# Kernel optimization log

Measured on AMD Instinct MI355X. Metric: run time of the kernel, lower is better.

The kernel has to match this reference:

```python
import jax, jax.numpy as jnp
import numpy as np

D = 1024           # d_model
E = 8              # n_experts
H = 2752           # hidden = round_up64(round(1024 * 8/3))
N = 8192
ALPHA = 0.05       # load_balance_alpha
TEMP = 1.0         # router temperature


def setup_inputs() -> dict:
    key = jax.random.key(0)
    k0, k1, k2, k3, k4 = jax.random.split(key, 5)
    s_in = 1.0 / np.sqrt(D)   # kaiming-uniform-ish bound for Linear(in=D)
    s_h = 1.0 / np.sqrt(H)    # bound for down proj Linear(in=H)
    x = jax.random.normal(k0, (N, D), jnp.float32)
    Wg = jax.random.uniform(k1, (E, D), jnp.float32, -s_in, s_in)   # router weight [E, D]
    bg = jnp.zeros((E,), jnp.float32)                               # router bias
    Wu = jax.random.uniform(k2, (E, H, D), jnp.float32, -s_in, s_in)  # up_u weights (torch [out,in])
    Wv = jax.random.uniform(k3, (E, H, D), jnp.float32, -s_in, s_in)  # up_v weights
    Wd = jax.random.uniform(k4, (E, D, H), jnp.float32, -s_h, s_h)    # down weights
    return {"x": x, "Wg": Wg, "bg": bg, "Wu": Wu, "Wv": Wv, "Wd": Wd}


def reference(x, Wg, bg, Wu, Wv, Wd):
    # ---- Top-1 router (eval mode: no noise, temperature=1) ----
    logits = x @ Wg.T + bg                 # [N, E]
    logits_base = logits / TEMP
    probs = jax.nn.softmax(logits_base, axis=-1)
    top1_idx = jnp.argmax(logits_base, axis=-1)                          # [N]
    top1_p = jnp.take_along_axis(probs, top1_idx[:, None], axis=-1)[:, 0]  # [N]

    # Load-balance aux loss (both factors are no-grad in the torch code)
    me = jax.lax.stop_gradient(jnp.mean(jax.nn.one_hot(top1_idx, E, dtype=probs.dtype), axis=0))
    ce = jax.lax.stop_gradient(jnp.mean(probs, axis=0))
    aux = ALPHA * E * jnp.sum(me * ce)

    # ---- Dropless dispatch + per-expert SwiGLU + weighted combine ----
    # Loop over the small, fixed expert set; each token contributes only via
    # its selected expert (gate is zero elsewhere), matching masked dispatch.
    y = jnp.zeros_like(x)
    for e in range(E):
        u = x @ Wu[e].T                    # [N, H]
        v = x @ Wv[e].T                    # [N, H]
        ye = (jax.nn.silu(u) * v) @ Wd[e].T  # [N, D]
        gate = jnp.where(top1_idx == e, top1_p, 0.0)  # [N]
        y = y + ye * gate[:, None]
    return y, aux
```

## Files before the change

### kernel.cpp

```cpp
#include <hip/hip_runtime.h>
#include <hip/hip_bf16.h>

#define NTOK 8192
#define DMODEL 1024
#define NEXP 8
#define HID 2752
#define ALPHA 0.05f

#define BM 128
#define BN 128
#define BK 64
#define MAXTILES 72

typedef __attribute__((ext_vector_type(8))) short bf16x8;
typedef __attribute__((ext_vector_type(8))) unsigned short u16x8;
typedef __attribute__((ext_vector_type(4))) unsigned short u16x4;
typedef __attribute__((ext_vector_type(4))) float f32x4;

__device__ __forceinline__ unsigned short f2bf(float f){
  unsigned u = __builtin_bit_cast(unsigned, f);
  u += 0x7fffu + ((u >> 16) & 1u);
  return (unsigned short)(u >> 16);
}

__device__ __forceinline__ void gload16(const void* g, void* l){
  __builtin_amdgcn_global_load_lds(
      (const __attribute__((address_space(1))) unsigned int*)g,
      (__attribute__((address_space(3))) unsigned int*)l, 16, 0, 0);
}

__global__ void k_init(int* counts, int* cursor, float* ce_sum){
  int t = threadIdx.x;
  if (t < NEXP){ counts[t] = 0; cursor[t] = 0; ce_sum[t] = 0.f; }
}

__global__ __launch_bounds__(1024) void k_router(
    const float* __restrict__ x, const float* __restrict__ Wg,
    const float* __restrict__ bg, int* __restrict__ counts,
    float* __restrict__ ce_sum, int* __restrict__ top1, float* __restrict__ gate,
    unsigned short* __restrict__ xb)
{
  __shared__ float wg[NEXP*DMODEL];
  __shared__ float ce_blk[NEXP];
  __shared__ int   cnt_blk[NEXP];
  const int tid = threadIdx.x;
  for (int i = tid; i < NEXP*DMODEL; i += 1024) wg[i] = Wg[i];
  if (tid < NEXP){ ce_blk[tid] = 0.f; cnt_blk[tid] = 0; }
  __syncthreads();
  const int wave = tid >> 6, lane = tid & 63;
  const int t = blockIdx.x * 16 + wave;
  float acc[NEXP];
  #pragma unroll
  for (int e = 0; e < NEXP; e++) acc[e] = 0.f;
  const float* xr = x + (size_t)t * DMODEL;
  unsigned short* xbr = xb + (size_t)t * DMODEL;
  #pragma unroll
  for (int kb = 0; kb < DMODEL; kb += 256){
    const float4 xv = *(const float4*)(xr + kb + lane*4);
    u16x4 o; o[0]=f2bf(xv.x); o[1]=f2bf(xv.y); o[2]=f2bf(xv.z); o[3]=f2bf(xv.w);
    *(u16x4*)(xbr + kb + lane*4) = o;
    #pragma unroll
    for (int e = 0; e < NEXP; e++){
      const float4 wv = *(const float4*)(wg + e*DMODEL + kb + lane*4);
      acc[e] += xv.x*wv.x + xv.y*wv.y + xv.z*wv.z + xv.w*wv.w;
    }
  }
  #pragma unroll
  for (int e = 0; e < NEXP; e++){
    float v = acc[e];
    #pragma unroll
    for (int off = 32; off; off >>= 1) v += __shfl_xor(v, off);
    acc[e] = v;
  }
  if (lane == 0){
    float mx = -1e30f; int bi = 0;
    float lg[NEXP];
    #pragma unroll
    for (int e = 0; e < NEXP; e++){
      lg[e] = acc[e] + bg[e];
      if (lg[e] > mx){ mx = lg[e]; bi = e; }
    }
    float s = 0.f, p[NEXP];
    #pragma unroll
    for (int e = 0; e < NEXP; e++){ p[e] = __expf(lg[e]-mx); s += p[e]; }
    const float inv = 1.f/s;
    #pragma unroll
    for (int e = 0; e < NEXP; e++) atomicAdd(&ce_blk[e], p[e]*inv);
    top1[t] = bi;
    gate[t] = p[bi]*inv;
    atomicAdd(&cnt_blk[bi], 1);
  }
  __syncthreads();
  if (tid < NEXP){
    atomicAdd(&counts[tid], cnt_blk[tid]);
    atomicAdd(&ce_sum[tid], ce_blk[tid]);
  }
}

__global__ __launch_bounds__(256) void k_cvtw(
    const float* __restrict__ Wu, const float* __restrict__ Wv, const float* __restrict__ Wd,
    unsigned short* __restrict__ Wub, unsigned short* __restrict__ Wvb,
    unsigned short* __restrict__ Wdb, int w8)
{
  const int tot = 3*w8;
  for (size_t i = (size_t)blockIdx.x*256 + threadIdx.x; i < (size_t)tot; i += (size_t)2048*256){
    const float* s; unsigned short* d; size_t j;
    if (i < (size_t)w8)        { s = Wu; d = Wub; j = i; }
    else if (i < (size_t)2*w8) { s = Wv; d = Wvb; j = i - w8; }
    else                       { s = Wd; d = Wdb; j = i - 2*(size_t)w8; }
    const float4 a = ((const float4*)s)[j*2];
    const float4 b = ((const float4*)s)[j*2+1];
    u16x8 o;
    o[0]=f2bf(a.x); o[1]=f2bf(a.y); o[2]=f2bf(a.z); o[3]=f2bf(a.w);
    o[4]=f2bf(b.x); o[5]=f2bf(b.y); o[6]=f2bf(b.z); o[7]=f2bf(b.w);
    ((u16x8*)d)[j] = o;
  }
}

__global__ void k_scan(const int* __restrict__ counts, const float* __restrict__ ce_sum,
                       int* offsets, int* nTiles, int* tileE, int* tileBase, int* tileCnt,
                       float* aux_out)
{
  if (threadIdx.x == 0){
    int off = 0;
    for (int e = 0; e < NEXP; e++){ offsets[e] = off; off += counts[e]; }
    offsets[NEXP] = off;
    int nt = 0;
    for (int e = 0; e < NEXP; e++){
      for (int r = 0; r < counts[e]; r += BM){
        tileE[nt] = e;
        tileBase[nt] = offsets[e] + r;
        int rem = counts[e] - r;
        tileCnt[nt] = rem < BM ? rem : BM;
        nt++;
      }
    }
    *nTiles = nt;
    float aux = 0.f;
    for (int e = 0; e < NEXP; e++)
      aux += ((float)counts[e] / (float)NTOK) * (ce_sum[e] / (float)NTOK);
    aux_out[0] = ALPHA * (float)NEXP * aux;
  }
}

__global__ __launch_bounds__(256) void k_scatter(const int* __restrict__ top1,
                                                 int* cursor, const int* __restrict__ offsets,
                                                 int* __restrict__ perm)
{
  const int t = blockIdx.x*256 + threadIdx.x;
  const int e = top1[t];
  const int lane = threadIdx.x & 63;
  int slot = 0;
  #pragma unroll
  for (int ee = 0; ee < NEXP; ee++){
    unsigned long long mask = __ballot(e == ee);
    if (e == ee){
      int leader = __ffsll(mask) - 1;
      int nbelow = __popcll(mask & ((1ull << lane) - 1ull));
      int base = 0;
      if (lane == leader) base = atomicAdd(&cursor[ee], __popcll(mask));
      base = __shfl(base, leader);
      slot = offsets[ee] + base + nbelow;
    }
  }
  perm[slot] = t;
}


__global__ __launch_bounds__(256,2) void k_up16(
    const unsigned short* __restrict__ xb,
    const unsigned short* __restrict__ Wub, const unsigned short* __restrict__ Wvb,
    const int* __restrict__ perm,
    const int* __restrict__ nTiles, const int* __restrict__ tileE,
    const int* __restrict__ tileBase, const int* __restrict__ tileCnt,
    unsigned short* __restrict__ h)
{
  const int l     = ((int)blockIdx.x % 8) * 198 + (int)blockIdx.x / 8;
  const int tileI = l % 72;
  const int ncol0 = (l / 72) * BN;
  if (tileI >= *nTiles) return;
  const int e    = tileE[tileI];
  const int base = tileBase[tileI];
  const int cnt  = tileCnt[tileI];

  __shared__ __align__(16) unsigned short As [BM*BK];
  __shared__ __align__(16) unsigned short Bus[BN*BK];
  __shared__ __align__(16) unsigned short Bvs[BN*BK];

  const int tid = threadIdx.x;
  const int wv = tid >> 6, ln = tid & 63;

  const unsigned short* srcA[4];
  const unsigned short* srcU[4];
  const unsigned short* srcV[4];
  #pragma unroll
  for (int c = 0; c < 4; c++){
    const int r  = wv*32 + c*8 + (ln>>3);
    const int sp = (ln&7) ^ (r&7);
    const int ra = (r < cnt) ? r : (cnt-1);
    srcA[c] = xb + (size_t)perm[base + ra]*DMODEL + sp*8;
    int rb = ncol0 + r; if (rb >= HID) rb = HID-1;
    srcU[c] = Wub + ((size_t)e*HID + rb)*DMODEL + sp*8;
    srcV[c] = Wvb + ((size_t)e*HID + rb)*DMODEL + sp*8;
  }

  const int wm = (wv >> 1) * 64, wn = (wv & 1) * 64;
  const int fr = ln & 15, fq = ln >> 4;

  f32x4 accU[4][4], accV[4][4];
  #pragma unroll
  for (int m = 0; m < 4; m++)
    #pragma unroll
    for (int n = 0; n < 4; n++)
      #pragma unroll
      for (int j = 0; j < 4; j++){ accU[m][n][j] = 0.f; accV[m][n][j] = 0.f; }

  for (int kb = 0; kb < DMODEL; kb += BK){
    #pragma unroll
    for (int c = 0; c < 4; c++){
      const unsigned ldo = wv*4096 + c*1024;
      gload16(srcA[c] + kb, (char*)As  + ldo);
      gload16(srcU[c] + kb, (char*)Bus + ldo);
      gload16(srcV[c] + kb, (char*)Bvs + ldo);
    }
    __syncthreads();
    #pragma unroll
    for (int ks = 0; ks < 2; ks++){
      bf16x8 af[4], bu[4], bv[4];
      #pragma unroll
      for (int m = 0; m < 4; m++){
        int r = wm + m*16 + fr;
        af[m] = *(const bf16x8*)((const char*)As + r*128 + ((ks*64 + fq*16) ^ ((r&7)<<4)));
      }
      #pragma unroll
      for (int n = 0; n < 4; n++){
        int r = wn + n*16 + fr;
        bu[n] = *(const bf16x8*)((const char*)Bus + r*128 + ((ks*64 + fq*16) ^ ((r&7)<<4)));
        bv[n] = *(const bf16x8*)((const char*)Bvs + r*128 + ((ks*64 + fq*16) ^ ((r&7)<<4)));
      }
      #pragma unroll
      for (int m = 0; m < 4; m++)
        #pragma unroll
        for (int n = 0; n < 4; n++){
          accU[m][n] = __builtin_amdgcn_mfma_f32_16x16x32_bf16(af[m], bu[n], accU[m][n], 0,0,0);
          accV[m][n] = __builtin_amdgcn_mfma_f32_16x16x32_bf16(af[m], bv[n], accV[m][n], 0,0,0);
        }
    }
    __syncthreads();
  }
  #pragma unroll
  for (int m = 0; m < 4; m++)
    #pragma unroll
    for (int n = 0; n < 4; n++)
      #pragma unroll
      for (int j = 0; j < 4; j++){
        int r = wm + m*16 + fq*4 + j;
        int c = ncol0 + wn + n*16 + fr;
        if (r < cnt && c < HID){
          float u = accU[m][n][j], v = accV[m][n][j];
          float hv = (u / (1.f + __expf(-u))) * v;
          h[(size_t)(base + r)*HID + c] = f2bf(hv);
        }
      }
}

__global__ __launch_bounds__(256,2) void k_down16(
    const unsigned short* __restrict__ h, const unsigned short* __restrict__ Wdb,
    const int* __restrict__ perm, const float* __restrict__ gate,
    const int* __restrict__ nTiles, const int* __restrict__ tileE,
    const int* __restrict__ tileBase, const int* __restrict__ tileCnt,
    float* __restrict__ out)
{
  const int l     = ((int)blockIdx.x % 8) * 72 + (int)blockIdx.x / 8;
  const int tileI = l % 72;
  const int ncol0 = (l / 72) * BN;
  if (tileI >= *nTiles) return;
  const int e    = tileE[tileI];
  const int base = tileBase[tileI];
  const int cnt  = tileCnt[tileI];

  __shared__ __align__(16) unsigned short As[BM*BK];
  __shared__ __align__(16) unsigned short Bs[BM*BK];
  __shared__ int   tokL[BM];
  __shared__ float gateL[BM];

  const int tid = threadIdx.x;
  if (tid < BM){
    int rr = (tid < cnt) ? tid : 0;
    int tk = perm[base + rr];
    tokL[tid] = tk;
    gateL[tid] = gate[tk];
  }
  const int wv = tid >> 6, ln = tid & 63;

  const unsigned short* srcA[4];
  const unsigned short* srcB[4];
  #pragma unroll
  for (int c = 0; c < 4; c++){
    const int r  = wv*32 + c*8 + (ln>>3);
    const int sp = (ln&7) ^ (r&7);
    const int ra = (r < cnt) ? r : (cnt-1);
    srcA[c] = h + (size_t)(base + ra)*HID + sp*8;
    const int rb = ncol0 + r;
    srcB[c] = Wdb + ((size_t)e*DMODEL + rb)*HID + sp*8;
  }

  const int wm = (wv >> 1) * 64, wn = (wv & 1) * 64;
  const int fr = ln & 15, fq = ln >> 4;

  f32x4 acc[4][4];
  #pragma unroll
  for (int m = 0; m < 4; m++)
    #pragma unroll
    for (int n = 0; n < 4; n++)
      #pragma unroll
      for (int j = 0; j < 4; j++) acc[m][n][j] = 0.f;

  for (int kb = 0; kb < HID; kb += BK){
    #pragma unroll
    for (int c = 0; c < 4; c++){
      const unsigned ldo = wv*4096 + c*1024;
      gload16(srcA[c] + kb, (char*)As + ldo);
      gload16(srcB[c] + kb, (char*)Bs + ldo);
    }
    __syncthreads();
    #pragma unroll
    for (int ks = 0; ks < 2; ks++){
      bf16x8 af[4], bf[4];
      #pragma unroll
      for (int m = 0; m < 4; m++){
        int r = wm + m*16 + fr;
        af[m] = *(const bf16x8*)((const char*)As + r*128 + ((ks*64 + fq*16) ^ ((r&7)<<4)));
      }
      #pragma unroll
      for (int n = 0; n < 4; n++){
        int r = wn + n*16 + fr;
        bf[n] = *(const bf16x8*)((const char*)Bs + r*128 + ((ks*64 + fq*16) ^ ((r&7)<<4)));
      }
      #pragma unroll
      for (int m = 0; m < 4; m++)
        #pragma unroll
        for (int n = 0; n < 4; n++)
          acc[m][n] = __builtin_amdgcn_mfma_f32_16x16x32_bf16(af[m], bf[n], acc[m][n], 0,0,0);
    }
    __syncthreads();
  }
  #pragma unroll
  for (int m = 0; m < 4; m++)
    #pragma unroll
    for (int n = 0; n < 4; n++)
      #pragma unroll
      for (int j = 0; j < 4; j++){
        int r = wm + m*16 + fq*4 + j;
        int c = ncol0 + wn + n*16 + fr;
        if (r < cnt)
          out[(size_t)tokL[r]*DMODEL + c] = acc[m][n][j] * gateL[r];
      }
}

extern "C" void kernel_launch(void* const* d_in, const int* in_sizes, int n_in,
                              void* d_out, int out_size, void* d_ws, size_t ws_size,
                              hipStream_t stream)
{
  const float* x  = (const float*)d_in[0];
  const float* Wg = (const float*)d_in[1];
  const float* bg = (const float*)d_in[2];
  const float* Wu = (const float*)d_in[3];
  const float* Wv = (const float*)d_in[4];
  const float* Wd = (const float*)d_in[5];
  float* out = (float*)d_out;

  char* ws = (char*)d_ws;
  int*   counts   = (int*)(ws + 0);
  int*   cursor   = (int*)(ws + 32);
  int*   offsets  = (int*)(ws + 64);
  float* ce_sum   = (float*)(ws + 128);
  int*   nTiles   = (int*)(ws + 192);
  int*   tileE    = (int*)(ws + 256);
  int*   tileBase = (int*)(ws + 768);
  int*   tileCnt  = (int*)(ws + 1280);
  int*   top1     = (int*)(ws + 2048);
  float* gate     = (float*)(ws + 34816);
  int*   perm     = (int*)(ws + 67584);
  unsigned short* xb   = (unsigned short*)(ws + 100352);
  unsigned short* hbuf = (unsigned short*)(ws + 100352 + (size_t)NTOK*DMODEL*2);
  const size_t W_ELEMS = (size_t)NEXP*HID*DMODEL;
  const size_t baseW = 100352 + (size_t)NTOK*DMODEL*2 + (size_t)NTOK*HID*2;
  unsigned short* Wub = (unsigned short*)(ws + baseW);
  unsigned short* Wvb = (unsigned short*)(ws + baseW + W_ELEMS*2);
  unsigned short* Wdb = (unsigned short*)(ws + baseW + W_ELEMS*4);

  k_init<<<1, 64, 0, stream>>>(counts, cursor, ce_sum);
  k_router<<<NTOK/16, 1024, 0, stream>>>(x, Wg, bg, counts, ce_sum, top1, gate, xb);
  k_scan<<<1, 64, 0, stream>>>(counts, ce_sum, offsets, nTiles, tileE, tileBase, tileCnt,
                               out + (size_t)NTOK*DMODEL);
  k_scatter<<<NTOK/256, 256, 0, stream>>>(top1, cursor, offsets, perm);
  k_cvtw<<<2048, 256, 0, stream>>>(Wu, Wv, Wd, Wub, Wvb, Wdb, (int)(W_ELEMS/8));

  k_up16<<<MAXTILES*((HID + BN - 1)/BN), 256, 0, stream>>>(
      xb, Wub, Wvb, perm, nTiles, tileE, tileBase, tileCnt, hbuf);
  k_down16<<<MAXTILES*(DMODEL/BN), 256, 0, stream>>>(
      hbuf, Wdb, perm, gate, nTiles, tileE, tileBase, tileCnt, out);
}
```

Baseline: 346.2 us.

## Double-buffer up-projection GEMM with BK=32 stages and async prefetch

Restructures the k_up16 main loop from a single-buffered BK=64 load-then-compute pattern into a two-stage LDS ring of BK=32 slices. The next slice's global-to-LDS loads are issued right after the fragment reads, so they overlap with the MFMA work, and explicit vmcnt/lgkmcnt waits and raw barriers replace __syncthreads. MFMA priority is raised with s_setprio, and the LDS swizzle is changed to match the 64-byte row pitch. This hides global load latency at the cost of more barriers per K step and hand-tuned waitcnt logic that has to stay consistent with the number of outstanding loads.

```diff
diff --git a/kernel.cpp b/kernel.cpp
--- a/kernel.cpp
+++ b/kernel.cpp
@@ -167,6 +167,14 @@
 }
 
 
+#define STG(AB, BB, CB, ofs) { \
+  gload16(srcA[0]+(ofs), (char*)(AB) + ldo); \
+  gload16(srcA[1]+(ofs), (char*)(AB) + 4096 + ldo); \
+  gload16(srcU[0]+(ofs), (char*)(BB) + ldo); \
+  gload16(srcU[1]+(ofs), (char*)(BB) + 4096 + ldo); \
+  gload16(srcV[0]+(ofs), (char*)(CB) + ldo); \
+  gload16(srcV[1]+(ofs), (char*)(CB) + 4096 + ldo); }
+
 __global__ __launch_bounds__(256,2) void k_up16(
     const unsigned short* __restrict__ xb,
     const unsigned short* __restrict__ Wub, const unsigned short* __restrict__ Wvb,
@@ -183,26 +191,27 @@
   const int base = tileBase[tileI];
   const int cnt  = tileCnt[tileI];
 
-  __shared__ __align__(16) unsigned short As [BM*BK];
-  __shared__ __align__(16) unsigned short Bus[BN*BK];
-  __shared__ __align__(16) unsigned short Bvs[BN*BK];
+  __shared__ __align__(16) unsigned short As [2][BM*32];
+  __shared__ __align__(16) unsigned short Bus[2][BM*32];
+  __shared__ __align__(16) unsigned short Bvs[2][BM*32];
 
   const int tid = threadIdx.x;
   const int wv = tid >> 6, ln = tid & 63;
 
-  const unsigned short* srcA[4];
-  const unsigned short* srcU[4];
-  const unsigned short* srcV[4];
-  #pragma unroll
-  for (int c = 0; c < 4; c++){
-    const int r  = wv*32 + c*8 + (ln>>3);
-    const int sp = (ln&7) ^ (r&7);
+  const unsigned short* srcA[2];
+  const unsigned short* srcU[2];
+  const unsigned short* srcV[2];
+  #pragma unroll
+  for (int c = 0; c < 2; c++){
+    const int r  = c*64 + wv*16 + (ln>>2);
+    const int sp = (ln&3) ^ ((r>>1)&3);
     const int ra = (r < cnt) ? r : (cnt-1);
     srcA[c] = xb + (size_t)perm[base + ra]*DMODEL + sp*8;
     int rb = ncol0 + r; if (rb >= HID) rb = HID-1;
     srcU[c] = Wub + ((size_t)e*HID + rb)*DMODEL + sp*8;
     srcV[c] = Wvb + ((size_t)e*HID + rb)*DMODEL + sp*8;
   }
+  const unsigned ldo = wv*1024;
 
   const int wm = (wv >> 1) * 64, wn = (wv & 1) * 64;
   const int fr = ln & 15, fq = ln >> 4;
@@ -215,39 +224,46 @@
       #pragma unroll
       for (int j = 0; j < 4; j++){ accU[m][n][j] = 0.f; accV[m][n][j] = 0.f; }
 
-  for (int kb = 0; kb < DMODEL; kb += BK){
-    #pragma unroll
-    for (int c = 0; c < 4; c++){
-      const unsigned ldo = wv*4096 + c*1024;
-      gload16(srcA[c] + kb, (char*)As  + ldo);
-      gload16(srcU[c] + kb, (char*)Bus + ldo);
-      gload16(srcV[c] + kb, (char*)Bvs + ldo);
-    }
-    __syncthreads();
-    #pragma unroll
-    for (int ks = 0; ks < 2; ks++){
-      bf16x8 af[4], bu[4], bv[4];
-      #pragma unroll
-      for (int m = 0; m < 4; m++){
-        int r = wm + m*16 + fr;
-        af[m] = *(const bf16x8*)((const char*)As + r*128 + ((ks*64 + fq*16) ^ ((r&7)<<4)));
-      }
+  STG(As[0], Bus[0], Bvs[0], 0);
+  STG(As[1], Bus[1], Bvs[1], 32);
+  asm volatile("s_waitcnt vmcnt(6)" ::: "memory");
+  __builtin_amdgcn_s_barrier();
+
+  #pragma unroll 2
+  for (int t = 0; t < 32; ++t){
+    const int bb = t & 1;
+    bf16x8 af[4], bu[4], bv[4];
+    #pragma unroll
+    for (int m = 0; m < 4; m++){
+      int r = wm + m*16 + fr;
+      int off = r*64 + ((fq ^ ((r>>1)&3))<<4);
+      af[m] = *(const bf16x8*)((const char*)As[bb] + off);
+    }
+    #pragma unroll
+    for (int n = 0; n < 4; n++){
+      int r = wn + n*16 + fr;
+      int off = r*64 + ((fq ^ ((r>>1)&3))<<4);
+      bu[n] = *(const bf16x8*)((const char*)Bus[bb] + off);
+      bv[n] = *(const bf16x8*)((const char*)Bvs[bb] + off);
+    }
+    asm volatile("s_waitcnt lgkmcnt(0)" ::: "memory");
+    __builtin_amdgcn_sched_barrier(0);
+    __builtin_amdgcn_s_barrier();
+    if (t < 30) STG(As[bb], Bus[bb], Bvs[bb], (t+2)*32);
+    __builtin_amdgcn_s_setprio(1);
+    #pragma unroll
+    for (int m = 0; m < 4; m++)
       #pragma unroll
       for (int n = 0; n < 4; n++){
-        int r = wn + n*16 + fr;
-        bu[n] = *(const bf16x8*)((const char*)Bus + r*128 + ((ks*64 + fq*16) ^ ((r&7)<<4)));
-        bv[n] = *(const bf16x8*)((const char*)Bvs + r*128 + ((ks*64 + fq*16) ^ ((r&7)<<4)));
-      }
-      #pragma unroll
-      for (int m = 0; m < 4; m++)
-        #pragma unroll
-        for (int n = 0; n < 4; n++){
-          accU[m][n] = __builtin_amdgcn_mfma_f32_16x16x32_bf16(af[m], bu[n], accU[m][n], 0,0,0);
-          accV[m][n] = __builtin_amdgcn_mfma_f32_16x16x32_bf16(af[m], bv[n], accV[m][n], 0,0,0);
-        }
-    }
-    __syncthreads();
-  }
+        accU[m][n] = __builtin_amdgcn_mfma_f32_16x16x32_bf16(af[m], bu[n], accU[m][n], 0,0,0);
+        accV[m][n] = __builtin_amdgcn_mfma_f32_16x16x32_bf16(af[m], bv[n], accV[m][n], 0,0,0);
+      }
+    __builtin_amdgcn_s_setprio(0);
+    if (t < 30)       { asm volatile("s_waitcnt vmcnt(6)" ::: "memory"); }
+    else if (t == 30) { asm volatile("s_waitcnt vmcnt(0)" ::: "memory"); }
+    if (t < 31) __builtin_amdgcn_s_barrier();
+  }
+
   #pragma unroll
   for (int m = 0; m < 4; m++)
     #pragma unroll
```

Measured after the change: 343.1 us. About the same (-0.9%).

## Widen up-projection tile to 256 columns with 512-thread blocks

Applied to the files above, without the earlier changes.

Rewrites the up-projection GEMM to use 128x256 output tiles per block with 8 waves, so each loaded A (token) tile is reused across twice as many hidden columns. The block now uses 80 KB of dynamic shared memory and runs at one block per CU. This cuts redundant activation loads and the block count, at the cost of less occupancy and a larger tail over the 2752-column dimension (11 tiles of 256, with the last one partly wasted).

```diff
diff --git a/kernel.cpp b/kernel.cpp
--- a/kernel.cpp
+++ b/kernel.cpp
@@ -166,8 +166,7 @@
   perm[slot] = t;
 }
 
-
-__global__ __launch_bounds__(256,2) void k_up16(
+__global__ __launch_bounds__(512,1) void k_up256(
     const unsigned short* __restrict__ xb,
     const unsigned short* __restrict__ Wub, const unsigned short* __restrict__ Wvb,
     const int* __restrict__ perm,
@@ -175,36 +174,44 @@
     const int* __restrict__ tileBase, const int* __restrict__ tileCnt,
     unsigned short* __restrict__ h)
 {
-  const int l     = ((int)blockIdx.x % 8) * 198 + (int)blockIdx.x / 8;
+  const int l     = ((int)blockIdx.x % 8) * 99 + (int)blockIdx.x / 8;
   const int tileI = l % 72;
-  const int ncol0 = (l / 72) * BN;
+  const int ncol0 = (l / 72) * 256;
   if (tileI >= *nTiles) return;
   const int e    = tileE[tileI];
   const int base = tileBase[tileI];
   const int cnt  = tileCnt[tileI];
 
-  __shared__ __align__(16) unsigned short As [BM*BK];
-  __shared__ __align__(16) unsigned short Bus[BN*BK];
-  __shared__ __align__(16) unsigned short Bvs[BN*BK];
+  extern __shared__ __align__(16) unsigned short smem[];
+  unsigned short* As  = smem;
+  unsigned short* Bus = smem + 128*64;
+  unsigned short* Bvs = smem + 128*64 + 256*64;
 
   const int tid = threadIdx.x;
   const int wv = tid >> 6, ln = tid & 63;
 
-  const unsigned short* srcA[4];
+  const unsigned short* srcA[2];
   const unsigned short* srcU[4];
   const unsigned short* srcV[4];
   #pragma unroll
-  for (int c = 0; c < 4; c++){
-    const int r  = wv*32 + c*8 + (ln>>3);
+  for (int c = 0; c < 2; c++){
+    const int r  = c*64 + wv*8 + (ln>>3);
     const int sp = (ln&7) ^ (r&7);
     const int ra = (r < cnt) ? r : (cnt-1);
     srcA[c] = xb + (size_t)perm[base + ra]*DMODEL + sp*8;
+  }
+  #pragma unroll
+  for (int c = 0; c < 4; c++){
+    const int r  = c*64 + wv*8 + (ln>>3);
+    const int sp = (ln&7) ^ (r&7);
     int rb = ncol0 + r; if (rb >= HID) rb = HID-1;
     srcU[c] = Wub + ((size_t)e*HID + rb)*DMODEL + sp*8;
     srcV[c] = Wvb + ((size_t)e*HID + rb)*DMODEL + sp*8;
   }
-
-  const int wm = (wv >> 1) * 64, wn = (wv & 1) * 64;
+  const unsigned ldo = wv*1024;
+
+  const int wm = (wv >> 2) * 64;
+  const int wn = (wv & 3) * 64;
   const int fr = ln & 15, fq = ln >> 4;
 
   f32x4 accU[4][4], accV[4][4];
@@ -217,11 +224,12 @@
 
   for (int kb = 0; kb < DMODEL; kb += BK){
     #pragma unroll
+    for (int c = 0; c < 2; c++)
+      gload16(srcA[c] + kb, (char*)As + c*8192 + ldo);
+    #pragma unroll
     for (int c = 0; c < 4; c++){
-      const unsigned ldo = wv*4096 + c*1024;
-      gload16(srcA[c] + kb, (char*)As  + ldo);
-      gload16(srcU[c] + kb, (char*)Bus + ldo);
-      gload16(srcV[c] + kb, (char*)Bvs + ldo);
+      gload16(srcU[c] + kb, (char*)Bus + c*8192 + ldo);
+      gload16(srcV[c] + kb, (char*)Bvs + c*8192 + ldo);
     }
     __syncthreads();
     #pragma unroll
@@ -397,7 +405,7 @@
   k_scatter<<<NTOK/256, 256, 0, stream>>>(top1, cursor, offsets, perm);
   k_cvtw<<<2048, 256, 0, stream>>>(Wu, Wv, Wd, Wub, Wvb, Wdb, (int)(W_ELEMS/8));
 
-  k_up16<<<MAXTILES*((HID + BN - 1)/BN), 256, 0, stream>>>(
+  k_up256<<<MAXTILES*11, 512, 80*1024, stream>>>(
       xb, Wub, Wvb, perm, nTiles, tileE, tileBase, tileCnt, hbuf);
   k_down16<<<MAXTILES*(DMODEL/BN), 256, 0, stream>>>(
       hbuf, Wdb, perm, gate, nTiles, tileE, tileBase, tileCnt, out);
```

After: 383.7 us. 1.11x slower.

## Load weight fragments directly from global memory into registers, bypassing LDS

Applied to the files above, without the earlier changes.

Both the up and down GEMM kernels stop staging the weight (B) tiles in shared memory. Each lane now reads its MFMA B fragments straight from global memory, and only the activation tile goes through LDS. This cuts LDS traffic and footprint, which may allow more resident blocks. The cost is that the B data is no longer shared across the waves that need it, so global and L2 reads grow. The global loads also sit in the MFMA inner loop with no prefetch, so their latency is exposed there.

```diff
diff --git a/kernel.cpp b/kernel.cpp
--- a/kernel.cpp
+++ b/kernel.cpp
@@ -183,30 +183,32 @@
   const int base = tileBase[tileI];
   const int cnt  = tileCnt[tileI];
 
-  __shared__ __align__(16) unsigned short As [BM*BK];
-  __shared__ __align__(16) unsigned short Bus[BN*BK];
-  __shared__ __align__(16) unsigned short Bvs[BN*BK];
+  __shared__ __align__(16) unsigned short As[BM*BK];
 
   const int tid = threadIdx.x;
   const int wv = tid >> 6, ln = tid & 63;
 
   const unsigned short* srcA[4];
-  const unsigned short* srcU[4];
-  const unsigned short* srcV[4];
   #pragma unroll
   for (int c = 0; c < 4; c++){
     const int r  = wv*32 + c*8 + (ln>>3);
     const int sp = (ln&7) ^ (r&7);
     const int ra = (r < cnt) ? r : (cnt-1);
     srcA[c] = xb + (size_t)perm[base + ra]*DMODEL + sp*8;
-    int rb = ncol0 + r; if (rb >= HID) rb = HID-1;
-    srcU[c] = Wub + ((size_t)e*HID + rb)*DMODEL + sp*8;
-    srcV[c] = Wvb + ((size_t)e*HID + rb)*DMODEL + sp*8;
   }
 
   const int wm = (wv >> 1) * 64, wn = (wv & 1) * 64;
   const int fr = ln & 15, fq = ln >> 4;
 
+  const unsigned short* bU[4];
+  const unsigned short* bV[4];
+  #pragma unroll
+  for (int n = 0; n < 4; n++){
+    int rb = ncol0 + wn + n*16 + fr; if (rb >= HID) rb = HID-1;
+    bU[n] = Wub + ((size_t)e*HID + rb)*DMODEL + fq*8;
+    bV[n] = Wvb + ((size_t)e*HID + rb)*DMODEL + fq*8;
+  }
+
   f32x4 accU[4][4], accV[4][4];
   #pragma unroll
   for (int m = 0; m < 4; m++)
@@ -217,26 +219,21 @@
 
   for (int kb = 0; kb < DMODEL; kb += BK){
     #pragma unroll
-    for (int c = 0; c < 4; c++){
-      const unsigned ldo = wv*4096 + c*1024;
-      gload16(srcA[c] + kb, (char*)As  + ldo);
-      gload16(srcU[c] + kb, (char*)Bus + ldo);
-      gload16(srcV[c] + kb, (char*)Bvs + ldo);
-    }
+    for (int c = 0; c < 4; c++)
+      gload16(srcA[c] + kb, (char*)As + wv*4096 + c*1024);
     __syncthreads();
     #pragma unroll
     for (int ks = 0; ks < 2; ks++){
-      bf16x8 af[4], bu[4], bv[4];
+      bf16x8 bu[4], bv[4], af[4];
+      #pragma unroll
+      for (int n = 0; n < 4; n++){
+        bu[n] = *(const bf16x8*)(bU[n] + kb + ks*32);
+        bv[n] = *(const bf16x8*)(bV[n] + kb + ks*32);
+      }
       #pragma unroll
       for (int m = 0; m < 4; m++){
         int r = wm + m*16 + fr;
         af[m] = *(const bf16x8*)((const char*)As + r*128 + ((ks*64 + fq*16) ^ ((r&7)<<4)));
-      }
-      #pragma unroll
-      for (int n = 0; n < 4; n++){
-        int r = wn + n*16 + fr;
-        bu[n] = *(const bf16x8*)((const char*)Bus + r*128 + ((ks*64 + fq*16) ^ ((r&7)<<4)));
-        bv[n] = *(const bf16x8*)((const char*)Bvs + r*128 + ((ks*64 + fq*16) ^ ((r&7)<<4)));
       }
       #pragma unroll
       for (int m = 0; m < 4; m++)
@@ -280,7 +277,6 @@
   const int cnt  = tileCnt[tileI];
 
   __shared__ __align__(16) unsigned short As[BM*BK];
-  __shared__ __align__(16) unsigned short Bs[BM*BK];
   __shared__ int   tokL[BM];
   __shared__ float gateL[BM];
 
@@ -294,20 +290,24 @@
   const int wv = tid >> 6, ln = tid & 63;
 
   const unsigned short* srcA[4];
-  const unsigned short* srcB[4];
   #pragma unroll
   for (int c = 0; c < 4; c++){
     const int r  = wv*32 + c*8 + (ln>>3);
     const int sp = (ln&7) ^ (r&7);
     const int ra = (r < cnt) ? r : (cnt-1);
     srcA[c] = h + (size_t)(base + ra)*HID + sp*8;
-    const int rb = ncol0 + r;
-    srcB[c] = Wdb + ((size_t)e*DMODEL + rb)*HID + sp*8;
   }
 
   const int wm = (wv >> 1) * 64, wn = (wv & 1) * 64;
   const int fr = ln & 15, fq = ln >> 4;
 
+  const unsigned short* bD[4];
+  #pragma unroll
+  for (int n = 0; n < 4; n++){
+    const int rb = ncol0 + wn + n*16 + fr;
+    bD[n] = Wdb + ((size_t)e*DMODEL + rb)*HID + fq*8;
+  }
+
   f32x4 acc[4][4];
   #pragma unroll
   for (int m = 0; m < 4; m++)
@@ -318,24 +318,19 @@
 
   for (int kb = 0; kb < HID; kb += BK){
     #pragma unroll
-    for (int c = 0; c < 4; c++){
-      const unsigned ldo = wv*4096 + c*1024;
-      gload16(srcA[c] + kb, (char*)As + ldo);
-      gload16(srcB[c] + kb, (char*)Bs + ldo);
-    }
+    for (int c = 0; c < 4; c++)
+      gload16(srcA[c] + kb, (char*)As + wv*4096 + c*1024);
     __syncthreads();
     #pragma unroll
     for (int ks = 0; ks < 2; ks++){
-      bf16x8 af[4], bf[4];
+      bf16x8 bf[4], af[4];
+      #pragma unroll
+      for (int n = 0; n < 4; n++)
+        bf[n] = *(const bf16x8*)(bD[n] + kb + ks*32);
       #pragma unroll
       for (int m = 0; m < 4; m++){
         int r = wm + m*16 + fr;
         af[m] = *(const bf16x8*)((const char*)As + r*128 + ((ks*64 + fq*16) ^ ((r&7)<<4)));
-      }
-      #pragma unroll
-      for (int n = 0; n < 4; n++){
-        int r = wn + n*16 + fr;
-        bf[n] = *(const bf16x8*)((const char*)Bs + r*128 + ((ks*64 + fq*16) ^ ((r&7)<<4)));
       }
       #pragma unroll
       for (int m = 0; m < 4; m++)
```

Result: slower. 523.0 us (+51.1%).
